# Kernel tuning notes

Hardware: AMD Instinct MI355X
Metric: run time of the kernel (lower is better)

Reference implementation:

```python
import jax, jax.numpy as jnp
import numpy as np

B, S, H, E, V, P = 64, 1024, 512, 512, 32000, 40


def setup_inputs() -> dict:
    key = jax.random.key(0)
    ks = jax.random.split(key, 18)
    s = 0.05  # weight scale to keep tanh/sigmoid in active range
    inp = {}
    inp["input_token"] = jax.random.randint(ks[0], (B,), 0, V, dtype=jnp.int32)
    inp["hidden"] = jax.random.normal(ks[1], (1, B, H), jnp.float32)
    inp["cell"] = jax.random.normal(ks[2], (1, B, H), jnp.float32)
    inp["encoder_outputs"] = jax.random.normal(ks[3], (B, S, H), jnp.float32)
    pos_ids = jax.random.randint(ks[4], (B, S), 0, P)
    inp["pos_onehot"] = jax.nn.one_hot(pos_ids, P, dtype=jnp.float32)
    inp["src_mask"] = jnp.zeros((B, S), dtype=bool)  # no PAD (avoids all -inf rows)
    # learned parameters (torch Linear convention: y = x @ W.T + b)
    inp["embed_table"] = jax.random.normal(ks[5], (V, E), jnp.float32) * s
    inp["W_s"] = jax.random.normal(ks[6], (H, H), jnp.float32) * s
    inp["W_h"] = jax.random.normal(ks[7], (H, H), jnp.float32) * s
    inp["V_w"] = jax.random.normal(ks[8], (H,), jnp.float32) * s
    inp["W_p"] = jax.random.normal(ks[9], (P,), jnp.float32) * s
    inp["b_p"] = jax.random.normal(ks[10], (), jnp.float32) * s
    inp["W_ih"] = jax.random.normal(ks[11], (4 * H, E + H), jnp.float32) * s
    inp["W_hh"] = jax.random.normal(ks[12], (4 * H, H), jnp.float32) * s
    inp["b_ih"] = jax.random.normal(ks[13], (4 * H,), jnp.float32) * s
    inp["b_hh"] = jax.random.normal(ks[14], (4 * H,), jnp.float32) * s
    inp["W_out"] = jax.random.normal(ks[15], (V, H), jnp.float32) * s
    inp["b_out"] = jax.random.normal(ks[16], (V,), jnp.float32) * s
    return inp


def reference(input_token, hidden, cell, encoder_outputs, pos_onehot, src_mask,
              embed_table, W_s, W_h, V_w, W_p, b_p,
              W_ih, W_hh, b_ih, b_hh, W_out, b_out):
    # embedding (dropout is identity in eval)
    emb = embed_table[input_token]                                  # (B, E)
    q = hidden[-1]                                                  # (B, H)
    # POS-gated Bahdanau attention
    qs = q @ W_s.T                                                  # (B, H)
    eh = jnp.einsum('bsh,kh->bsk', encoder_outputs, W_h)            # (B, S, H)
    energy = jnp.tanh(qs[:, None, :] + eh)                          # (B, S, H)
    scores = jnp.einsum('bsh,h->bs', energy, V_w)                   # (B, S)
    gate = jax.nn.sigmoid(pos_onehot @ W_p + b_p)                   # (B, S)
    gated = jnp.where(src_mask, jnp.float32(-1e30), scores * gate)
    attn = jax.nn.softmax(gated, axis=-1)                           # (B, S)
    context = jnp.einsum('bs,bsh->bh', attn, encoder_outputs)       # (B, H)
    # single-step, single-layer LSTM (torch gate order: i, f, g, o)
    lstm_in = jnp.concatenate([emb, context], axis=-1)              # (B, E+H)
    gates = lstm_in @ W_ih.T + hidden[0] @ W_hh.T + b_ih + b_hh     # (B, 4H)
    i, f, g, o = jnp.split(gates, 4, axis=-1)
    c1 = jax.nn.sigmoid(f) * cell[0] + jax.nn.sigmoid(i) * jnp.tanh(g)
    h1 = jax.nn.sigmoid(o) * jnp.tanh(c1)                           # (B, H)
    pred = h1 @ W_out.T + b_out                                     # (B, V)
    return (pred, h1[None], c1[None], attn)
```

## Files before the change

### kernel.cpp

```cpp
#include <hip/hip_runtime.h>

#define BB 64
#define SS 1024
#define HH 512
#define EE 512
#define VV 32000
#define PP 40

typedef __attribute__((ext_vector_type(8))) __bf16 bf16x8;
typedef __attribute__((ext_vector_type(4))) float f32x4;
typedef __attribute__((ext_vector_type(8))) unsigned short us8_t;
typedef __attribute__((ext_vector_type(4))) unsigned short us4_t;

__device__ inline float fast_tanh(float x) {
    float e = __expf(-2.0f * fabsf(x));
    float t = (1.0f - e) / (1.0f + e);
    return copysignf(t, x);
}
__device__ inline float sigmf(float x) { return 1.0f / (1.0f + __expf(-x)); }

__device__ inline unsigned int cvtpk(float lo, float hi) {
    unsigned int r;
    asm volatile("v_cvt_pk_bf16_f32 %0, %1, %2" : "=v"(r) : "v"(lo), "v"(hi));
    return r;
}
__device__ inline us8_t pack8c(float4 x, float4 y) {
    union { unsigned int u[4]; us8_t v; } r;
    r.u[0] = cvtpk(x.x, x.y); r.u[1] = cvtpk(x.z, x.w);
    r.u[2] = cvtpk(y.x, y.y); r.u[3] = cvtpk(y.z, y.w);
    return r.v;
}

__global__ __launch_bounds__(256)
void k_prep(const float* __restrict__ hidden, const float* __restrict__ Ws,
            const float* __restrict__ Wh, const float* __restrict__ pos,
            const float* __restrict__ Wp, const float* __restrict__ bp,
            unsigned short* __restrict__ wh16, float* __restrict__ qs,
            float* __restrict__ gate, float* __restrict__ ctx) {
    int blk = blockIdx.x, t = threadIdx.x;
    if (blk < 64) {
        __shared__ float hb[HH];
        int b = blk;
        for (int i = t; i < HH; i += 256) hb[i] = hidden[b * HH + i];
        __syncthreads();
        for (int n = t; n < HH; n += 256) {
            const float* wr = Ws + (size_t)n * HH;
            float acc = 0.0f;
#pragma unroll 4
            for (int k = 0; k < HH; k += 4) {
                float4 w = *(const float4*)(wr + k);
                acc += w.x * hb[k] + w.y * hb[k + 1] + w.z * hb[k + 2] + w.w * hb[k + 3];
            }
            qs[b * HH + n] = acc;
        }
    } else if (blk < 96) {
        int base = (blk - 64) * 8192 + t * 4;
#pragma unroll
        for (int j = 0; j < 8; ++j) {
            int idx = base + j * 1024;
            float4 x = *(const float4*)(Wh + idx);
            union { unsigned int u[2]; us4_t v; } r;
            r.u[0] = cvtpk(x.x, x.y); r.u[1] = cvtpk(x.z, x.w);
            *(us4_t*)(wh16 + idx) = r.v;
        }
    } else if (blk < 352) {
        int idx = (blk - 96) * 256 + t;
        const float* pr = pos + (size_t)idx * PP;
        float acc = bp[0];
#pragma unroll
        for (int j = 0; j < 10; ++j) {
            float4 x = *(const float4*)(pr + j * 4);
            acc += x.x * Wp[j * 4] + x.y * Wp[j * 4 + 1] + x.z * Wp[j * 4 + 2] + x.w * Wp[j * 4 + 3];
        }
        gate[idx] = sigmf(acc);
    } else {
        int idx = (blk - 352) * 256 + t;
#pragma unroll
        for (int j = 0; j < 16; ++j) ctx[idx * 16 + j] = 0.0f;
    }
}

__global__ __launch_bounds__(512)
__attribute__((amdgpu_waves_per_eu(2, 2)))
void k_scores(const float* __restrict__ enc, const unsigned short* __restrict__ wh16,
              const float* __restrict__ qs, const float* __restrict__ Vw,
              float* __restrict__ part) {
    __shared__ unsigned short tile[2][8192];
    __shared__ float pbuf[8][128];
    int bid = blockIdx.x;
    int nh = bid >> 9, rest = bid & 511;
    int b = rest >> 3, sc = rest & 7;
    int s0 = sc * 128;
    int w = threadIdx.x >> 6, lane = threadIdx.x & 63;
    int l15 = lane & 15, lq = lane >> 4;
    int n0w = nh * 256 + w * 32;

    us8_t areg[2][16];
    const unsigned short* abase = wh16 + (size_t)(n0w + l15) * 512 + lq * 8;
#pragma unroll
    for (int nf = 0; nf < 2; ++nf)
#pragma unroll
        for (int ks = 0; ks < 16; ++ks) {
            areg[nf][ks] = *(const us8_t*)(abase + nf * 16 * 512 + ks * 32);
            asm volatile("" : "+v"(areg[nf][ks]));
        }

    float qv[2][4], vw[2][4];
#pragma unroll
    for (int nf = 0; nf < 2; ++nf)
#pragma unroll
        for (int r = 0; r < 4; ++r) {
            int n = n0w + nf * 16 + lq * 4 + r;
            qv[nf][r] = qs[b * HH + n];
            vw[nf][r] = Vw[n];
        }

    int sr = threadIdx.x >> 5, seg = threadIdx.x & 31;
    const float* gsrc = enc + ((size_t)(b * SS + s0 + sr)) * HH + seg * 16;
    int slot1 = (seg >> 1) * 4 + (seg & 1) * 2;
    int off1 = slot1 * 128 + ((sr ^ (slot1 & 15)) & 15) * 8;
    int off2 = (slot1 + 1) * 128 + ((sr ^ ((slot1 + 1) & 15)) & 15) * 8;

    float4 x0 = *(const float4*)(gsrc);
    float4 x1 = *(const float4*)(gsrc + 4);
    float4 x2 = *(const float4*)(gsrc + 8);
    float4 x3 = *(const float4*)(gsrc + 12);
    *(us8_t*)(tile[0] + off1) = pack8c(x0, x1);
    *(us8_t*)(tile[0] + off2) = pack8c(x2, x3);
    {
        const float* g = gsrc + (size_t)16 * HH;
        x0 = *(const float4*)(g);
        x1 = *(const float4*)(g + 4);
        x2 = *(const float4*)(g + 8);
        x3 = *(const float4*)(g + 12);
    }
    asm volatile("s_waitcnt lgkmcnt(0)" ::: "memory");
    __builtin_amdgcn_s_barrier();

#pragma unroll
    for (int st = 0; st < 8; ++st) {
        float4 y0, y1, y2, y3;
        if (st < 6) {
            const float* g = gsrc + (size_t)(st + 2) * 16 * HH;
            y0 = *(const float4*)(g);
            y1 = *(const float4*)(g + 4);
            y2 = *(const float4*)(g + 8);
            y3 = *(const float4*)(g + 12);
        }
        const unsigned short* tb = tile[st & 1];
        f32x4 acc0 = {0.f, 0.f, 0.f, 0.f};
        f32x4 acc1 = {0.f, 0.f, 0.f, 0.f};
#pragma unroll
        for (int ks = 0; ks < 16; ++ks) {
            int u = ks * 4 + lq;
            us8_t bf = *(const us8_t*)(tb + u * 128 + ((l15 ^ (u & 15)) & 15) * 8);
            acc0 = __builtin_amdgcn_mfma_f32_16x16x32_bf16(
                __builtin_bit_cast(bf16x8, areg[0][ks]),
                __builtin_bit_cast(bf16x8, bf), acc0, 0, 0, 0);
            acc1 = __builtin_amdgcn_mfma_f32_16x16x32_bf16(
                __builtin_bit_cast(bf16x8, areg[1][ks]),
                __builtin_bit_cast(bf16x8, bf), acc1, 0, 0, 0);
        }
        float p = 0.0f;
#pragma unroll
        for (int r = 0; r < 4; ++r) {
            p += fast_tanh(acc0[r] + qv[0][r]) * vw[0][r];
            p += fast_tanh(acc1[r] + qv[1][r]) * vw[1][r];
        }
        p += __shfl_xor(p, 16, 64);
        p += __shfl_xor(p, 32, 64);
        if (lq == 0) pbuf[w][st * 16 + l15] = p;

        if (st < 7) {
            unsigned short* tn = (unsigned short*)tile[(st + 1) & 1];
            *(us8_t*)(tn + off1) = pack8c(x0, x1);
            *(us8_t*)(tn + off2) = pack8c(x2, x3);
        }
        asm volatile("s_waitcnt lgkmcnt(0)" ::: "memory");
        __builtin_amdgcn_s_barrier();
        if (st < 6) { x0 = y0; x1 = y1; x2 = y2; x3 = y3; }
    }

    if (threadIdx.x < 128) {
        float s = 0.0f;
#pragma unroll
        for (int ww = 0; ww < 8; ++ww) s += pbuf[ww][threadIdx.x];
        part[nh * (BB * SS) + b * SS + s0 + threadIdx.x] = s;
    }
}

__global__ __launch_bounds__(256)
void k_context(const float* __restrict__ enc, const float* __restrict__ part,
               const float* __restrict__ gate, const unsigned char* __restrict__ mask,
               float* __restrict__ attn, float* __restrict__ ctx) {
    int b = blockIdx.x >> 4, chunk = blockIdx.x & 15;
    int s0 = chunk * 64, t = threadIdx.x;
    int w = t >> 6, ln = t & 63;
    float sum = 0.0f;
#pragma unroll
    for (int j = 0; j < 4; ++j) {
        int s = j * 256 + t;
        float raw = part[b * SS + s] + part[BB * SS + b * SS + s];
        float v = mask[b * SS + s] ? -1e30f : raw * gate[b * SS + s];
        sum += __expf(v);
    }
#pragma unroll
    for (int off = 1; off < 64; off <<= 1) sum += __shfl_xor(sum, off, 64);
    __shared__ float sl[4];
    if (ln == 0) sl[w] = sum;
    __syncthreads();
    float inv = 1.0f / (sl[0] + sl[1] + sl[2] + sl[3]);

    __shared__ float aw[64];
    if (t < 64) {
        int s = s0 + t;
        float raw = part[b * SS + s] + part[BB * SS + b * SS + s];
        float v = mask[b * SS + s] ? -1e30f : raw * gate[b * SS + s];
        float a = __expf(v) * inv;
        aw[t] = a;
        attn[b * SS + s] = a;
    }
    __syncthreads();

    const float* eb = enc + ((size_t)(b * SS + s0)) * HH + 2 * t;
    float a0 = 0.f, a1 = 0.f;
#pragma unroll 4
    for (int s = 0; s < 64; ++s) {
        float2 u = *(const float2*)(eb + (size_t)s * HH);
        a0 += aw[s] * u.x;
        a1 += aw[s] * u.y;
    }
    atomicAdd(&ctx[b * HH + 2 * t], a0);
    atomicAdd(&ctx[b * HH + 2 * t + 1], a1);
}

__global__ __launch_bounds__(256)
void k_build(const int* __restrict__ tok, const float* __restrict__ embt,
             const float* __restrict__ ctx, const float* __restrict__ hidden,
             unsigned short* __restrict__ li16, unsigned short* __restrict__ h16v) {
    int b = blockIdx.x, t = threadIdx.x;
    const float* er = embt + (size_t)tok[b] * EE;
    for (int i = 2 * t; i < HH; i += 512) {
        *(unsigned int*)(li16 + b * 1024 + i) = cvtpk(er[i], er[i + 1]);
        *(unsigned int*)(li16 + b * 1024 + 512 + i) = cvtpk(ctx[b * HH + i], ctx[b * HH + i + 1]);
        *(unsigned int*)(h16v + b * HH + i) = cvtpk(hidden[b * HH + i], hidden[b * HH + i + 1]);
    }
}

__global__ __launch_bounds__(256)
void k_gates(const unsigned short* __restrict__ li16, const unsigned short* __restrict__ h16v,
             const float* __restrict__ Wih, const float* __restrict__ Whh,
             float* __restrict__ gpart) {
    int nt = blockIdx.x >> 2, ksl = blockIdx.x & 3;
    int wave = threadIdx.x >> 6, lane = threadIdx.x & 63;
    int l15 = lane & 15, lq = lane >> 4, k0 = lq * 8;
    int n0w = nt * 128 + wave * 32;
    f32x4 acc[4][2];
#pragma unroll
    for (int mf = 0; mf < 4; ++mf)
#pragma unroll
        for (int nf = 0; nf < 2; ++nf) acc[mf][nf] = (f32x4){0.f, 0.f, 0.f, 0.f};

    for (int ks = 0; ks < 12; ++ks) {
        int kg = ksl * 384 + ks * 32;
        us8_t af[4];
        if (kg < 1024) {
#pragma unroll
            for (int mf = 0; mf < 4; ++mf)
                af[mf] = *(const us8_t*)(li16 + (mf * 16 + l15) * 1024 + kg + k0);
        } else {
#pragma unroll
            for (int mf = 0; mf < 4; ++mf)
                af[mf] = *(const us8_t*)(h16v + (mf * 16 + l15) * 512 + (kg - 1024) + k0);
        }
#pragma unroll
        for (int nf = 0; nf < 2; ++nf) {
            int n = n0w + nf * 16 + l15;
            us8_t bu;
            if (kg < 1024) {
                const float* wr = Wih + (size_t)n * 1024 + kg + k0;
                bu = pack8c(*(const float4*)wr, *(const float4*)(wr + 4));
            } else {
                const float* wr = Whh + (size_t)n * 512 + (kg - 1024) + k0;
                bu = pack8c(*(const float4*)wr, *(const float4*)(wr + 4));
            }
#pragma unroll
            for (int mf = 0; mf < 4; ++mf)
                acc[mf][nf] = __builtin_amdgcn_mfma_f32_16x16x32_bf16(
                    __builtin_bit_cast(bf16x8, af[mf]),
                    __builtin_bit_cast(bf16x8, bu), acc[mf][nf], 0, 0, 0);
        }
    }
#pragma unroll
    for (int mf = 0; mf < 4; ++mf)
#pragma unroll
        for (int nf = 0; nf < 2; ++nf)
#pragma unroll
            for (int r = 0; r < 4; ++r) {
                int row = mf * 16 + lq * 4 + r;
                int n = n0w + nf * 16 + l15;
                gpart[ksl * (BB * 2048) + row * 2048 + n] = acc[mf][nf][r];
            }
}

__global__ __launch_bounds__(512)
void k_lstm(const float* __restrict__ gpart, const float* __restrict__ bih,
            const float* __restrict__ bhh, const float* __restrict__ cell,
            float* __restrict__ oh, float* __restrict__ oc,
            unsigned short* __restrict__ h116) {
    int b = blockIdx.x, t = threadIdx.x;
    float gi = bih[t] + bhh[t];
    float gf = bih[512 + t] + bhh[512 + t];
    float gg = bih[1024 + t] + bhh[1024 + t];
    float go = bih[1536 + t] + bhh[1536 + t];
#pragma unroll
    for (int ksl = 0; ksl < 4; ++ksl) {
        const float* gp = gpart + ksl * (BB * 2048) + b * 2048;
        gi += gp[t];
        gf += gp[512 + t];
        gg += gp[1024 + t];
        go += gp[1536 + t];
    }
    float c0 = cell[b * HH + t];
    float c1 = sigmf(gf) * c0 + sigmf(gi) * fast_tanh(gg);
    float h1 = sigmf(go) * fast_tanh(c1);
    oh[b * HH + t] = h1;
    oc[b * HH + t] = c1;
    h116[b * HH + t] = (unsigned short)(cvtpk(h1, h1) & 0xffffu);
}

__global__ __launch_bounds__(512)
void k_pred(const unsigned short* __restrict__ h116, const float* __restrict__ Wout,
            const float* __restrict__ bout, float* __restrict__ pred) {
    int wave = threadIdx.x >> 6, lane = threadIdx.x & 63;
    int l15 = lane & 15, lq = lane >> 4, k0 = lq * 8;
    int n = blockIdx.x * 128 + wave * 16 + l15;
    f32x4 acc[4];
#pragma unroll
    for (int mf = 0; mf < 4; ++mf) acc[mf] = (f32x4){0.f, 0.f, 0.f, 0.f};
    const float* wr = Wout + (size_t)n * HH;
#pragma unroll 4
    for (int ks = 0; ks < 16; ++ks) {
        float4 x = *(const float4*)(wr + ks * 32 + k0);
        float4 y = *(const float4*)(wr + ks * 32 + k0 + 4);
        us8_t bu = pack8c(x, y);
#pragma unroll
        for (int mf = 0; mf < 4; ++mf) {
            us8_t au = *(const us8_t*)(h116 + (mf * 16 + l15) * 512 + ks * 32 + k0);
            acc[mf] = __builtin_amdgcn_mfma_f32_16x16x32_bf16(
                __builtin_bit_cast(bf16x8, au),
                __builtin_bit_cast(bf16x8, bu), acc[mf], 0, 0, 0);
        }
    }
    float bo = bout[n];
#pragma unroll
    for (int mf = 0; mf < 4; ++mf)
#pragma unroll
        for (int r = 0; r < 4; ++r) {
            int row = mf * 16 + lq * 4 + r;
            pred[(size_t)row * VV + n] = acc[mf][r] + bo;
        }
}

extern "C" void kernel_launch(void* const* d_in, const int* in_sizes, int n_in,
                              void* d_out, int out_size, void* d_ws, size_t ws_size,
                              hipStream_t stream) {
    const int* tok = (const int*)d_in[0];
    const float* hidden = (const float*)d_in[1];
    const float* cell = (const float*)d_in[2];
    const float* enc = (const float*)d_in[3];
    const float* pos = (const float*)d_in[4];
    const unsigned char* mask = (const unsigned char*)d_in[5];
    const float* embt = (const float*)d_in[6];
    const float* Ws = (const float*)d_in[7];
    const float* Wh = (const float*)d_in[8];
    const float* Vw = (const float*)d_in[9];
    const float* Wp = (const float*)d_in[10];
    const float* bp = (const float*)d_in[11];
    const float* Wih = (const float*)d_in[12];
    const float* Whh = (const float*)d_in[13];
    const float* bih = (const float*)d_in[14];
    const float* bhh = (const float*)d_in[15];
    const float* Wout = (const float*)d_in[16];
    const float* bout = (const float*)d_in[17];

    float* out = (float*)d_out;
    float* pred = out;
    float* out_h = out + 2048000;
    float* out_c = out + 2080768;
    float* attn = out + 2113536;

    char* wsb = (char*)d_ws;
    unsigned short* wh16 = (unsigned short*)(wsb);
    float* qs = (float*)(wsb + (512 << 10));
    float* gate = (float*)(wsb + (640 << 10));
    float* part = (float*)(wsb + (896 << 10));
    float* ctx = (float*)(wsb + (1408 << 10));
    unsigned short* li16 = (unsigned short*)(wsb + (1536 << 10));
    unsigned short* h16v = (unsigned short*)(wsb + (1664 << 10));
    float* gpart = (float*)(wsb + (1728 << 10));
    unsigned short* h116 = (unsigned short*)(wsb + (3776 << 10));

    hipLaunchKernelGGL(k_prep, dim3(360), dim3(256), 0, stream,
                       hidden, Ws, Wh, pos, Wp, bp, wh16, qs, gate, ctx);
    hipLaunchKernelGGL(k_scores, dim3(1024), dim3(512), 0, stream,
                       enc, wh16, qs, Vw, part);
    hipLaunchKernelGGL(k_context, dim3(1024), dim3(256), 0, stream,
                       enc, part, gate, mask, attn, ctx);
    hipLaunchKernelGGL(k_build, dim3(64), dim3(256), 0, stream,
                       tok, embt, ctx, hidden, li16, h16v);
    hipLaunchKernelGGL(k_gates, dim3(64), dim3(256), 0, stream, li16, h16v, Wih, Whh, gpart);
    hipLaunchKernelGGL(k_lstm, dim3(64), dim3(512), 0, stream,
                       gpart, bih, bhh, cell, out_h, out_c, h116);
    hipLaunchKernelGGL(k_pred, dim3(250), dim3(512), 0, stream, h116, Wout, bout, pred);
}
```

Before: 190.9 us.

## Restructure attention score GEMM into a 2D-tiled K-loop with register accumulators

Replaces the scheme where each wave held its W_h slice in registers and streamed encoder rows through swizzled LDS. The new kernel stages both encoder (bf16-converted) and W_h tiles per 32-wide K step into padded LDS, with a 2x4 wave grid each computing a 64x64 block of 4x4 MFMA accumulators. The tanh/V reduction now runs once at the end with intra-row shuffles. This raises MFMA operand reuse per LDS read but adds 16 K-steps with two barriers each, and the waves_per_eu hint is dropped.

```diff
diff --git a/kernel.cpp b/kernel.cpp
--- a/kernel.cpp
+++ b/kernel.cpp
@@ -81,111 +81,117 @@
 }
 
 __global__ __launch_bounds__(512)
-__attribute__((amdgpu_waves_per_eu(2, 2)))
 void k_scores(const float* __restrict__ enc, const unsigned short* __restrict__ wh16,
               const float* __restrict__ qs, const float* __restrict__ Vw,
               float* __restrict__ part) {
-    __shared__ unsigned short tile[2][8192];
-    __shared__ float pbuf[8][128];
+    __shared__ unsigned short As[128 * 40];
+    __shared__ unsigned short Bs[256 * 40];
+    __shared__ float pbuf[4][128];
     int bid = blockIdx.x;
     int nh = bid >> 9, rest = bid & 511;
     int b = rest >> 3, sc = rest & 7;
-    int s0 = sc * 128;
-    int w = threadIdx.x >> 6, lane = threadIdx.x & 63;
+    int s0 = sc * 128, n0 = nh * 256;
+    int tid = threadIdx.x;
+    int w = tid >> 6, lane = tid & 63;
+    int wm = w >> 2, wn = w & 3;
     int l15 = lane & 15, lq = lane >> 4;
-    int n0w = nh * 256 + w * 32;
-
-    us8_t areg[2][16];
-    const unsigned short* abase = wh16 + (size_t)(n0w + l15) * 512 + lq * 8;
-#pragma unroll
-    for (int nf = 0; nf < 2; ++nf)
-#pragma unroll
-        for (int ks = 0; ks < 16; ++ks) {
-            areg[nf][ks] = *(const us8_t*)(abase + nf * 16 * 512 + ks * 32);
-            asm volatile("" : "+v"(areg[nf][ks]));
-        }
-
-    float qv[2][4], vw[2][4];
-#pragma unroll
-    for (int nf = 0; nf < 2; ++nf)
-#pragma unroll
-        for (int r = 0; r < 4; ++r) {
-            int n = n0w + nf * 16 + lq * 4 + r;
-            qv[nf][r] = qs[b * HH + n];
-            vw[nf][r] = Vw[n];
-        }
-
-    int sr = threadIdx.x >> 5, seg = threadIdx.x & 31;
-    const float* gsrc = enc + ((size_t)(b * SS + s0 + sr)) * HH + seg * 16;
-    int slot1 = (seg >> 1) * 4 + (seg & 1) * 2;
-    int off1 = slot1 * 128 + ((sr ^ (slot1 & 15)) & 15) * 8;
-    int off2 = (slot1 + 1) * 128 + ((sr ^ ((slot1 + 1) & 15)) & 15) * 8;
-
-    float4 x0 = *(const float4*)(gsrc);
-    float4 x1 = *(const float4*)(gsrc + 4);
-    float4 x2 = *(const float4*)(gsrc + 8);
-    float4 x3 = *(const float4*)(gsrc + 12);
-    *(us8_t*)(tile[0] + off1) = pack8c(x0, x1);
-    *(us8_t*)(tile[0] + off2) = pack8c(x2, x3);
+
+    float qv[4], vw[4];
+#pragma unroll
+    for (int nf = 0; nf < 4; ++nf) {
+        int n = n0 + wn * 64 + nf * 16 + l15;
+        qv[nf] = qs[b * HH + n];
+        vw[nf] = Vw[n];
+    }
+
+    int ar = tid >> 2, akseg = tid & 3;
+    const float* aSrc = enc + ((size_t)(b * SS + s0 + ar)) * HH + akseg * 8;
+    int br = tid >> 1, bkseg = tid & 1;
+    const unsigned short* bSrc = wh16 + (size_t)(n0 + br) * HH + bkseg * 16;
+    int aOff = ar * 40 + akseg * 8;
+    int bOff = br * 40 + bkseg * 16;
+
+    int aRd[4], bRd[4];
+#pragma unroll
+    for (int mf = 0; mf < 4; ++mf) aRd[mf] = (wm * 64 + mf * 16 + l15) * 40 + lq * 8;
+#pragma unroll
+    for (int nf = 0; nf < 4; ++nf) bRd[nf] = (wn * 64 + nf * 16 + l15) * 40 + lq * 8;
+
+    f32x4 acc[4][4];
+#pragma unroll
+    for (int mf = 0; mf < 4; ++mf)
+#pragma unroll
+        for (int nf = 0; nf < 4; ++nf) acc[mf][nf] = (f32x4){0.f, 0.f, 0.f, 0.f};
+
     {
-        const float* g = gsrc + (size_t)16 * HH;
-        x0 = *(const float4*)(g);
-        x1 = *(const float4*)(g + 4);
-        x2 = *(const float4*)(g + 8);
-        x3 = *(const float4*)(g + 12);
-    }
+        float4 a0 = *(const float4*)(aSrc);
+        float4 a1 = *(const float4*)(aSrc + 4);
+        us8_t b0 = *(const us8_t*)(bSrc);
+        us8_t b1 = *(const us8_t*)(bSrc + 8);
+        *(us8_t*)(As + aOff) = pack8c(a0, a1);
+        *(us8_t*)(Bs + bOff) = b0;
+        *(us8_t*)(Bs + bOff + 8) = b1;
+    }
+    float4 xa0 = *(const float4*)(aSrc + 32);
+    float4 xa1 = *(const float4*)(aSrc + 36);
+    us8_t xb0 = *(const us8_t*)(bSrc + 32);
+    us8_t xb1 = *(const us8_t*)(bSrc + 40);
     asm volatile("s_waitcnt lgkmcnt(0)" ::: "memory");
     __builtin_amdgcn_s_barrier();
 
 #pragma unroll
-    for (int st = 0; st < 8; ++st) {
-        float4 y0, y1, y2, y3;
-        if (st < 6) {
-            const float* g = gsrc + (size_t)(st + 2) * 16 * HH;
-            y0 = *(const float4*)(g);
-            y1 = *(const float4*)(g + 4);
-            y2 = *(const float4*)(g + 8);
-            y3 = *(const float4*)(g + 12);
-        }
-        const unsigned short* tb = tile[st & 1];
-        f32x4 acc0 = {0.f, 0.f, 0.f, 0.f};
-        f32x4 acc1 = {0.f, 0.f, 0.f, 0.f};
-#pragma unroll
-        for (int ks = 0; ks < 16; ++ks) {
-            int u = ks * 4 + lq;
-            us8_t bf = *(const us8_t*)(tb + u * 128 + ((l15 ^ (u & 15)) & 15) * 8);
-            acc0 = __builtin_amdgcn_mfma_f32_16x16x32_bf16(
-                __builtin_bit_cast(bf16x8, areg[0][ks]),
-                __builtin_bit_cast(bf16x8, bf), acc0, 0, 0, 0);
-            acc1 = __builtin_amdgcn_mfma_f32_16x16x32_bf16(
-                __builtin_bit_cast(bf16x8, areg[1][ks]),
-                __builtin_bit_cast(bf16x8, bf), acc1, 0, 0, 0);
-        }
-        float p = 0.0f;
-#pragma unroll
-        for (int r = 0; r < 4; ++r) {
-            p += fast_tanh(acc0[r] + qv[0][r]) * vw[0][r];
-            p += fast_tanh(acc1[r] + qv[1][r]) * vw[1][r];
-        }
-        p += __shfl_xor(p, 16, 64);
-        p += __shfl_xor(p, 32, 64);
-        if (lq == 0) pbuf[w][st * 16 + l15] = p;
-
-        if (st < 7) {
-            unsigned short* tn = (unsigned short*)tile[(st + 1) & 1];
-            *(us8_t*)(tn + off1) = pack8c(x0, x1);
-            *(us8_t*)(tn + off2) = pack8c(x2, x3);
-        }
+    for (int st = 0; st < 16; ++st) {
+        float4 ya0, ya1; us8_t yb0, yb1;
+        if (st < 14) {
+            const float* ga = aSrc + (st + 2) * 32;
+            ya0 = *(const float4*)(ga);
+            ya1 = *(const float4*)(ga + 4);
+            const unsigned short* gb = bSrc + (st + 2) * 32;
+            yb0 = *(const us8_t*)(gb);
+            yb1 = *(const us8_t*)(gb + 8);
+        }
+        us8_t af[4], bf[4];
+#pragma unroll
+        for (int mf = 0; mf < 4; ++mf) af[mf] = *(const us8_t*)(As + aRd[mf]);
+#pragma unroll
+        for (int nf = 0; nf < 4; ++nf) bf[nf] = *(const us8_t*)(Bs + bRd[nf]);
         asm volatile("s_waitcnt lgkmcnt(0)" ::: "memory");
         __builtin_amdgcn_s_barrier();
-        if (st < 6) { x0 = y0; x1 = y1; x2 = y2; x3 = y3; }
-    }
-
-    if (threadIdx.x < 128) {
-        float s = 0.0f;
-#pragma unroll
-        for (int ww = 0; ww < 8; ++ww) s += pbuf[ww][threadIdx.x];
-        part[nh * (BB * SS) + b * SS + s0 + threadIdx.x] = s;
+        if (st < 15) {
+            *(us8_t*)(As + aOff) = pack8c(xa0, xa1);
+            *(us8_t*)(Bs + bOff) = xb0;
+            *(us8_t*)(Bs + bOff + 8) = xb1;
+        }
+#pragma unroll
+        for (int mf = 0; mf < 4; ++mf)
+#pragma unroll
+            for (int nf = 0; nf < 4; ++nf)
+                acc[mf][nf] = __builtin_amdgcn_mfma_f32_16x16x32_bf16(
+                    __builtin_bit_cast(bf16x8, af[mf]),
+                    __builtin_bit_cast(bf16x8, bf[nf]), acc[mf][nf], 0, 0, 0);
+        asm volatile("s_waitcnt lgkmcnt(0)" ::: "memory");
+        __builtin_amdgcn_s_barrier();
+        if (st < 14) { xa0 = ya0; xa1 = ya1; xb0 = yb0; xb1 = yb1; }
+    }
+
+#pragma unroll
+    for (int mf = 0; mf < 4; ++mf)
+#pragma unroll
+        for (int r = 0; r < 4; ++r) {
+            float p = 0.0f;
+#pragma unroll
+            for (int nf = 0; nf < 4; ++nf)
+                p += vw[nf] * fast_tanh(acc[mf][nf][r] + qv[nf]);
+            p += __shfl_xor(p, 1, 64);
+            p += __shfl_xor(p, 2, 64);
+            p += __shfl_xor(p, 4, 64);
+            p += __shfl_xor(p, 8, 64);
+            if (l15 == 0) pbuf[wn][wm * 64 + mf * 16 + lq * 4 + r] = p;
+        }
+    __syncthreads();
+    if (tid < 128) {
+        part[nh * (BB * SS) + b * SS + s0 + tid] =
+            pbuf[0][tid] + pbuf[1][tid] + pbuf[2][tid] + pbuf[3][tid];
     }
 }
 
```

Measured after the change: 175.8 us. 1.09x faster.
